# Kernel optimization log

Hardware: AMD Instinct MI355X
Metric: run time of the kernel (lower is better)

The kernel has to match this reference:

```python
import jax, jax.numpy as jnp
import numpy as np

# Quantum circuit math: each wire starts in |0>, gets RX(x_i) (encoder), then a
# single-qubit, the n-wire state is a product state and each wire's <Z> is
# analytically cos(theta_i) * cos(x_i):
#   RX(x)|0> = [cos(x/2), -i sin(x/2)];  after RY(th):
#   <Z> = (cos^2(th/2)-sin^2(th/2)) * (cos^2(x/2)-sin^2(x/2)) = cos(th)cos(x).
# This is exactly the math the torchquantum simulator computes, expressed in
# closed form (no 2^d_k state vector needed).

NUM_HEADS = 64


def setup_inputs() -> dict:
    key = jax.random.key(0)
    k1, k2, k3 = jax.random.split(key, 3)
    B, T, E = 4, 1024, 512
    d_k = E // NUM_HEADS  # 8 wires
    x = jax.random.normal(k1, (B, T, E), dtype=jnp.float32)
    theta = jax.random.normal(k2, (d_k,), dtype=jnp.float32)  # shared RY params (one QLayer reused across heads)
    W_combine = jax.random.normal(k3, (E, E), dtype=jnp.float32) * (E ** -0.5)
    b_combine = jnp.zeros((E,), dtype=jnp.float32)
    return {"x": x, "theta": theta, "W_combine": W_combine, "b_combine": b_combine}


def reference(x, theta, W_combine, b_combine):
    B, T, E = x.shape
    H = NUM_HEADS
    d_k = E // H
    # split heads: [B, H, T, d_k]
    xh = x.reshape(B, T, H, d_k).transpose(0, 2, 1, 3)
    # quantum layer output: per-wire PauliZ expectation = cos(theta) * cos(x)
    proj = jnp.cos(xh) * jnp.cos(theta)  # [B, H, T, d_k]
    # self-attention on quantum projections
    scale = 1.0 / (d_k ** 0.5)
    scores = jnp.einsum('bhtd,bhsd->bhts', proj, proj) * scale  # [B, H, T, T]
    probs = jax.nn.softmax(scores, axis=-1)
    # dropout is identity in eval mode
    attn = jnp.einsum('bhts,bhsd->bhtd', probs, proj)  # [B, H, T, d_k]
    out = attn.transpose(0, 2, 1, 3).reshape(B, T, E)
    return out @ W_combine.T + b_combine
```

## Files before the change

kernel.cpp:

```cpp
#include <hip/hip_runtime.h>
#include <hip/hip_bf16.h>
#include <cstdint>
#include <cstddef>

#define T_DIM 1024
#define E_DIM 512

typedef short bf16x4 __attribute__((ext_vector_type(4)));
typedef short bf16x8 __attribute__((ext_vector_type(8)));
typedef float f32x4  __attribute__((ext_vector_type(4)));
typedef float f32x16 __attribute__((ext_vector_type(16)));

#if __has_builtin(__builtin_amdgcn_mfma_f32_32x32x8bf16_1k)
#define SCORE_K8 1
#else
#define SCORE_K8 0
#endif

__global__ __launch_bounds__(512, 4)
void qattn_mfma(const float* __restrict__ x,
                const float* __restrict__ theta,
                const float* __restrict__ W,
                __hip_bfloat16* __restrict__ attn_out,
                __hip_bfloat16* __restrict__ w_bf)
{
    __shared__ __align__(16) char shraw[16384 + 20640];
    auto projA = (__hip_bfloat16 (*)[8])(shraw);
    auto projT = (__hip_bfloat16 (*)[1032])(shraw + 16384);

    const int p    = blockIdx.x;
    const int xcd  = p & 7;
    const int idx  = p >> 3;
    const int head = xcd * 32 + (idx >> 1);
    const int qh   = idx & 1;
    const int b    = head >> 6;
    const int h    = head & 63;
    const int tid  = threadIdx.x;
    const int lane = tid & 63;
    const int wv   = tid >> 6;
    const int l31  = lane & 31;
    const int hf   = lane >> 5;

    {
        const int gid = p * 512 + tid;
        if (gid < 65536) {
            const float4 v = *(const float4*)(W + gid * 4);
            alignas(8) __hip_bfloat16 ob[4] = {
                __float2bfloat16(v.x), __float2bfloat16(v.y),
                __float2bfloat16(v.z), __float2bfloat16(v.w)};
            *(uint2*)(w_bf + gid * 4) = *(const uint2*)ob;
        }
    }

    const float SA2 = 8.0804315f;
    float ctT[8], ctA[8];
#pragma unroll
    for (int d = 0; d < 8; ++d) {
        ctT[d] = __cosf(theta[d]);
        ctA[d] = ctT[d] * SA2;
    }

    const float* xb = x + (size_t)b * T_DIM * E_DIM + h * 8;
    const float4 va0 = *(const float4*)(xb + (size_t)tid * E_DIM);
    const float4 va1 = *(const float4*)(xb + (size_t)tid * E_DIM + 4);
    const float4 vb0 = *(const float4*)(xb + (size_t)(tid + 512) * E_DIM);
    const float4 vb1 = *(const float4*)(xb + (size_t)(tid + 512) * E_DIM + 4);
#pragma unroll
    for (int rr = 0; rr < 2; ++rr) {
        const int r = tid + rr * 512;
        const float4 v0 = rr ? vb0 : va0;
        const float4 v1 = rr ? vb1 : va1;
        float pr[8] = {v0.x, v0.y, v0.z, v0.w, v1.x, v1.y, v1.z, v1.w};
        alignas(16) __hip_bfloat16 ra[8];
#pragma unroll
        for (int d = 0; d < 8; ++d) {
            const float c = __cosf(pr[d]);
            ra[d] = __float2bfloat16(c * ctA[d]);
            projT[d][r] = __float2bfloat16(c * ctT[d]);
        }
        *(uint4*)&projA[r][0] = *(const uint4*)ra;
        projT[8][r] = __ushort_as_bfloat16((unsigned short)0x3f80);
        projT[9][r] = __ushort_as_bfloat16((unsigned short)0);
    }
    __syncthreads();

    const float MAGIC = 8404858.0f;
    f32x16 cinit;
#pragma unroll
    for (int i = 0; i < 16; ++i) cinit[i] = MAGIC;

    const int q0 = qh * 512 + wv * 64;

#if SCORE_K8
    bf16x4 bq4[2];
#pragma unroll
    for (int qt = 0; qt < 2; ++qt)
        bq4[qt] = *(const bf16x4*)&projA[q0 + qt * 32 + l31][hf * 4];
    const __hip_bfloat16* kabase = &projA[l31][hf * 4];
#else
    const bf16x8 z8 = {};
    bf16x8 bq[2];
#pragma unroll
    for (int qt = 0; qt < 2; ++qt)
        bq[qt] = (hf == 0) ? *(const bf16x8*)&projA[q0 + qt * 32 + l31][0]
                           : z8;
    const __hip_bfloat16* kabase =
        (hf == 0) ? &projA[l31][0] : &projA[0][0];
#endif

    f32x16 nacc[2] = {};

    const int bvrow = (l31 < 8) ? l31 : ((l31 == 8) ? 8 : 9);
    const __hip_bfloat16* bvbase = &projT[bvrow][hf * 4];

#pragma unroll
    for (int kc = 0; kc < 32; ++kc) {
        const int key0 = kc * 32;
#if SCORE_K8
        const bf16x4 ka4 = *(const bf16x4*)(kabase + (size_t)key0 * 8);
#else
        const bf16x8 ka = *(const bf16x8*)(kabase + (size_t)key0 * 8);
#endif

        union { uint2 u[2]; bf16x8 v; } bA, bB;
        bA.u[0] = *(const uint2*)(bvbase + key0);
        bA.u[1] = *(const uint2*)(bvbase + key0 + 8);
        bB.u[0] = *(const uint2*)(bvbase + key0 + 16);
        bB.u[1] = *(const uint2*)(bvbase + key0 + 24);

#pragma unroll
        for (int qt = 0; qt < 2; ++qt) {
#if SCORE_K8
            const f32x16 s = __builtin_amdgcn_mfma_f32_32x32x8bf16_1k(
                ka4, bq4[qt], cinit, 0, 0, 0);
#else
            const f32x16 s = __builtin_amdgcn_mfma_f32_32x32x16_bf16(
                ka, bq[qt], cinit, 0, 0, 0);
#endif

            union { f32x16 f; uint32_t u[16]; } a;
            a.f = s;
            union { uint32_t u[4]; bf16x8 v; } pA, pB;
#pragma unroll
            for (int i = 0; i < 4; ++i) {
                pA.u[i] = __builtin_amdgcn_perm(a.u[2 * i + 1], a.u[2 * i],
                                                0x05040100u);
                pB.u[i] = __builtin_amdgcn_perm(a.u[8 + 2 * i + 1],
                                                a.u[8 + 2 * i], 0x05040100u);
            }
            nacc[qt] = __builtin_amdgcn_mfma_f32_32x32x16_bf16(
                pA.v, bA.v, nacc[qt], 0, 0, 0);
            nacc[qt] = __builtin_amdgcn_mfma_f32_32x32x16_bf16(
                pB.v, bB.v, nacc[qt], 0, 0, 0);
        }
    }

    const int denSrc = (lane & 32) | 8;
#pragma unroll
    for (int qt = 0; qt < 2; ++qt) {
#pragma unroll
        for (int r = 0; r < 16; ++r) {
            const float den = __shfl(nacc[qt][r], denSrc);
            const float inv = __builtin_amdgcn_rcpf(den);
            if (l31 < 8) {
                const int qrow = q0 + qt * 32 + (r & 3) + 8 * (r >> 2) + 4 * hf;
                attn_out[(size_t)(b * T_DIM + qrow) * E_DIM + h * 8 + l31] =
                    __float2bfloat16(nacc[qt][r] * inv);
            }
        }
    }
}

#define BM 64
#define BN 64
#define BK 64

__global__ __launch_bounds__(256, 2)
void combine_gemm(const __hip_bfloat16* __restrict__ A,
                  const __hip_bfloat16* __restrict__ Wb,
                  const float* __restrict__ bias,
                  float* __restrict__ out)
{
    __shared__ __hip_bfloat16 As[2][BM][BK];
    __shared__ __hip_bfloat16 Bs[2][BN][BK];

    const int tid  = threadIdx.x;
    const int lane = tid & 63;
    const int wave = tid >> 6;
    const int bm   = blockIdx.x;
    const int bn   = blockIdx.y;
    const int wm   = (wave & 1) * 32;
    const int wn   = (wave >> 1) * 32;
    const int rlo  = lane & 15;
    const int quad = lane >> 4;

    f32x4 acc[2][2] = {};

    auto stage = [&](int buf, int k0) {
#pragma unroll
        for (int pp = 0; pp < 2; ++pp) {
            const int c   = pp * 256 + tid;
            const int row = c >> 3;
            const int kcs = c & 7;
            const int kc  = kcs ^ (row & 7);
            const __hip_bfloat16* gA =
                A + (size_t)(bm * BM + row) * E_DIM + k0 + kc * 8;
            char* lA = (char*)&As[buf][0][0] +
                       (size_t)(pp * 256 + wave * 64) * 16;
            __builtin_amdgcn_global_load_lds(
                (const __attribute__((address_space(1))) void*)gA,
                (__attribute__((address_space(3))) void*)lA, 16, 0, 0);
        }
#pragma unroll
        for (int pp = 0; pp < 2; ++pp) {
            const int c   = pp * 256 + tid;
            const int row = c >> 3;
            const int kcs = c & 7;
            const int kc  = kcs ^ (row & 7);
            const __hip_bfloat16* gW =
                Wb + (size_t)(bn * BN + row) * E_DIM + k0 + kc * 8;
            char* lB = (char*)&Bs[buf][0][0] +
                       (size_t)(pp * 256 + wave * 64) * 16;
            __builtin_amdgcn_global_load_lds(
                (const __attribute__((address_space(1))) void*)gW,
                (__attribute__((address_space(3))) void*)lB, 16, 0, 0);
        }
    };

    stage(0, 0);
    __syncthreads();

#pragma unroll
    for (int t = 0; t < 8; ++t) {
        const int cb = t & 1;
        if (t + 1 < 8) stage(cb ^ 1, (t + 1) * BK);

#pragma unroll
        for (int ks = 0; ks < 2; ++ks) {
            const int kci  = ks * 4 + quad;
            const int koff = (kci ^ (rlo & 7)) * 8;
            bf16x8 af[2], bf[2];
#pragma unroll
            for (int i = 0; i < 2; ++i)
                af[i] = *(const bf16x8*)&As[cb][wm + i * 16 + rlo][koff];
#pragma unroll
            for (int j = 0; j < 2; ++j)
                bf[j] = *(const bf16x8*)&Bs[cb][wn + j * 16 + rlo][koff];
#pragma unroll
            for (int i = 0; i < 2; ++i)
#pragma unroll
                for (int j = 0; j < 2; ++j)
                    acc[i][j] = __builtin_amdgcn_mfma_f32_16x16x32_bf16(
                        af[i], bf[j], acc[i][j], 0, 0, 0);
        }
        __syncthreads();
    }

    const int row0 = bm * BM + wm;
    const int col0 = bn * BN + wn;
#pragma unroll
    for (int j = 0; j < 2; ++j) {
        const int col = col0 + j * 16 + rlo;
        const float bv = bias[col];
#pragma unroll
        for (int i = 0; i < 2; ++i) {
            const int rbase = row0 + i * 16 + quad * 4;
#pragma unroll
            for (int r = 0; r < 4; ++r)
                out[(size_t)(rbase + r) * E_DIM + col] = acc[i][j][r] + bv;
        }
    }
}

extern "C" void kernel_launch(void* const* d_in, const int* in_sizes, int n_in,
                              void* d_out, int out_size, void* d_ws,
                              size_t ws_size, hipStream_t stream)
{
    const float* x     = (const float*)d_in[0];
    const float* theta = (const float*)d_in[1];
    const float* W     = (const float*)d_in[2];
    const float* bias  = (const float*)d_in[3];
    float* out = (float*)d_out;

    __hip_bfloat16* attn_bf = (__hip_bfloat16*)d_ws;
    __hip_bfloat16* w_bf    = (__hip_bfloat16*)((char*)d_ws + 4u * 1024u * 1024u);

    hipLaunchKernelGGL(qattn_mfma, dim3(512), dim3(512), 0, stream,
                       x, theta, W, attn_bf, w_bf);
    hipLaunchKernelGGL(combine_gemm, dim3(64, 8), dim3(256), 0, stream,
                       attn_bf, w_bf, bias, out);
}
```

Before: 92.28 us.

## Overlap loading of other-half keys with attention on own-half keys

Each block now loads and projects only its own half of the sequence (the rows matching its query half) before the first barrier. It runs attention over those keys while loading and projecting the other half in two pieces, then syncs and processes the rest. The W-to-bf16 conversion is restricted to 128 threads per block. The aim is to hide global load latency and cosine work behind MFMA compute, at the cost of an extra barrier and a changed key-processing order.

```diff
diff --git a/kernel.cpp b/kernel.cpp
--- a/kernel.cpp
+++ b/kernel.cpp
@@ -41,15 +41,13 @@
     const int l31  = lane & 31;
     const int hf   = lane >> 5;
 
-    {
-        const int gid = p * 512 + tid;
-        if (gid < 65536) {
-            const float4 v = *(const float4*)(W + gid * 4);
-            alignas(8) __hip_bfloat16 ob[4] = {
-                __float2bfloat16(v.x), __float2bfloat16(v.y),
-                __float2bfloat16(v.z), __float2bfloat16(v.w)};
-            *(uint2*)(w_bf + gid * 4) = *(const uint2*)ob;
-        }
+    if (tid < 128) {
+        const int gid = p * 128 + tid;
+        const float4 v = *(const float4*)(W + gid * 4);
+        alignas(8) __hip_bfloat16 ob[4] = {
+            __float2bfloat16(v.x), __float2bfloat16(v.y),
+            __float2bfloat16(v.z), __float2bfloat16(v.w)};
+        *(uint2*)(w_bf + gid * 4) = *(const uint2*)ob;
     }
 
     const float SA2 = 8.0804315f;
@@ -61,15 +59,11 @@
     }
 
     const float* xb = x + (size_t)b * T_DIM * E_DIM + h * 8;
-    const float4 va0 = *(const float4*)(xb + (size_t)tid * E_DIM);
-    const float4 va1 = *(const float4*)(xb + (size_t)tid * E_DIM + 4);
-    const float4 vb0 = *(const float4*)(xb + (size_t)(tid + 512) * E_DIM);
-    const float4 vb1 = *(const float4*)(xb + (size_t)(tid + 512) * E_DIM + 4);
-#pragma unroll
-    for (int rr = 0; rr < 2; ++rr) {
-        const int r = tid + rr * 512;
-        const float4 v0 = rr ? vb0 : va0;
-        const float4 v1 = rr ? vb1 : va1;
+
+    {
+        const int r = qh * 512 + tid;
+        const float4 v0 = *(const float4*)(xb + (size_t)r * E_DIM);
+        const float4 v1 = *(const float4*)(xb + (size_t)r * E_DIM + 4);
         float pr[8] = {v0.x, v0.y, v0.z, v0.w, v1.x, v1.y, v1.z, v1.w};
         alignas(16) __hip_bfloat16 ra[8];
 #pragma unroll
@@ -79,8 +73,10 @@
             projT[d][r] = __float2bfloat16(c * ctT[d]);
         }
         *(uint4*)&projA[r][0] = *(const uint4*)ra;
-        projT[8][r] = __ushort_as_bfloat16((unsigned short)0x3f80);
-        projT[9][r] = __ushort_as_bfloat16((unsigned short)0);
+        projT[8][tid]       = __ushort_as_bfloat16((unsigned short)0x3f80);
+        projT[8][tid + 512] = __ushort_as_bfloat16((unsigned short)0x3f80);
+        projT[9][tid]       = __ushort_as_bfloat16((unsigned short)0);
+        projT[9][tid + 512] = __ushort_as_bfloat16((unsigned short)0);
     }
     __syncthreads();
 
@@ -113,47 +109,86 @@
     const int bvrow = (l31 < 8) ? l31 : ((l31 == 8) ? 8 : 9);
     const __hip_bfloat16* bvbase = &projT[bvrow][hf * 4];
 
-#pragma unroll
-    for (int kc = 0; kc < 32; ++kc) {
-        const int key0 = kc * 32;
+    auto computeChunk = [&](int cbase) {
+#pragma unroll
+        for (int j = 0; j < 8; ++j) {
+            const int key0 = cbase + j * 32;
 #if SCORE_K8
-        const bf16x4 ka4 = *(const bf16x4*)(kabase + (size_t)key0 * 8);
+            const bf16x4 ka4 = *(const bf16x4*)(kabase + (size_t)key0 * 8);
 #else
-        const bf16x8 ka = *(const bf16x8*)(kabase + (size_t)key0 * 8);
+            const bf16x8 ka = *(const bf16x8*)(kabase + (size_t)key0 * 8);
 #endif
-
-        union { uint2 u[2]; bf16x8 v; } bA, bB;
-        bA.u[0] = *(const uint2*)(bvbase + key0);
-        bA.u[1] = *(const uint2*)(bvbase + key0 + 8);
-        bB.u[0] = *(const uint2*)(bvbase + key0 + 16);
-        bB.u[1] = *(const uint2*)(bvbase + key0 + 24);
-
-#pragma unroll
-        for (int qt = 0; qt < 2; ++qt) {
+            union { uint2 u[2]; bf16x8 v; } bA, bB;
+            bA.u[0] = *(const uint2*)(bvbase + key0);
+            bA.u[1] = *(const uint2*)(bvbase + key0 + 8);
+            bB.u[0] = *(const uint2*)(bvbase + key0 + 16);
+            bB.u[1] = *(const uint2*)(bvbase + key0 + 24);
+
+#pragma unroll
+            for (int qt = 0; qt < 2; ++qt) {
 #if SCORE_K8
-            const f32x16 s = __builtin_amdgcn_mfma_f32_32x32x8bf16_1k(
-                ka4, bq4[qt], cinit, 0, 0, 0);
+                const f32x16 s = __builtin_amdgcn_mfma_f32_32x32x8bf16_1k(
+                    ka4, bq4[qt], cinit, 0, 0, 0);
 #else
-            const f32x16 s = __builtin_amdgcn_mfma_f32_32x32x16_bf16(
-                ka, bq[qt], cinit, 0, 0, 0);
+                const f32x16 s = __builtin_amdgcn_mfma_f32_32x32x16_bf16(
+                    ka, bq[qt], cinit, 0, 0, 0);
 #endif
-
-            union { f32x16 f; uint32_t u[16]; } a;
-            a.f = s;
-            union { uint32_t u[4]; bf16x8 v; } pA, pB;
-#pragma unroll
-            for (int i = 0; i < 4; ++i) {
-                pA.u[i] = __builtin_amdgcn_perm(a.u[2 * i + 1], a.u[2 * i],
-                                                0x05040100u);
-                pB.u[i] = __builtin_amdgcn_perm(a.u[8 + 2 * i + 1],
-                                                a.u[8 + 2 * i], 0x05040100u);
+                union { f32x16 f; uint32_t u[16]; } a;
+                a.f = s;
+                union { uint32_t u[4]; bf16x8 v; } pA, pB;
+#pragma unroll
+                for (int i = 0; i < 4; ++i) {
+                    pA.u[i] = __builtin_amdgcn_perm(a.u[2 * i + 1],
+                                                    a.u[2 * i], 0x05040100u);
+                    pB.u[i] = __builtin_amdgcn_perm(a.u[8 + 2 * i + 1],
+                                                    a.u[8 + 2 * i],
+                                                    0x05040100u);
+                }
+                nacc[qt] = __builtin_amdgcn_mfma_f32_32x32x16_bf16(
+                    pA.v, bA.v, nacc[qt], 0, 0, 0);
+                nacc[qt] = __builtin_amdgcn_mfma_f32_32x32x16_bf16(
+                    pB.v, bB.v, nacc[qt], 0, 0, 0);
             }
-            nacc[qt] = __builtin_amdgcn_mfma_f32_32x32x16_bf16(
-                pA.v, bA.v, nacc[qt], 0, 0, 0);
-            nacc[qt] = __builtin_amdgcn_mfma_f32_32x32x16_bf16(
-                pB.v, bB.v, nacc[qt], 0, 0, 0);
-        }
-    }
+        }
+    };
+
+    const int otherBase = (1 - qh) * 512;
+    const int prow = tid >> 1;
+    const int phh  = tid & 1;
+
+    {
+        const int r0 = otherBase + prow;
+        const float4 pv = *(const float4*)(xb + (size_t)r0 * E_DIM + phh * 4);
+        computeChunk(qh ? 512 : 0);
+        alignas(8) __hip_bfloat16 ra[4];
+        const float prf[4] = {pv.x, pv.y, pv.z, pv.w};
+#pragma unroll
+        for (int j = 0; j < 4; ++j) {
+            const int d = phh * 4 + j;
+            const float c = __cosf(prf[j]);
+            ra[j] = __float2bfloat16(c * ctA[d]);
+            projT[d][r0] = __float2bfloat16(c * ctT[d]);
+        }
+        *(uint2*)&projA[r0][phh * 4] = *(const uint2*)ra;
+    }
+    {
+        const int r1 = otherBase + 256 + prow;
+        const float4 pv = *(const float4*)(xb + (size_t)r1 * E_DIM + phh * 4);
+        computeChunk((qh ? 512 : 0) + 256);
+        alignas(8) __hip_bfloat16 ra[4];
+        const float prf[4] = {pv.x, pv.y, pv.z, pv.w};
+#pragma unroll
+        for (int j = 0; j < 4; ++j) {
+            const int d = phh * 4 + j;
+            const float c = __cosf(prf[j]);
+            ra[j] = __float2bfloat16(c * ctA[d]);
+            projT[d][r1] = __float2bfloat16(c * ctT[d]);
+        }
+        *(uint2*)&projA[r1][phh * 4] = *(const uint2*)ra;
+    }
+    __syncthreads();
+    computeChunk(otherBase);
+    computeChunk(otherBase + 256);
 
     const int denSrc = (lane & 32) | 8;
 #pragma unroll
```

Result: no change. 92.91 us (+0.7%).
